# Optimization experiments

Hardware: AMD Instinct MI355X
Metric: run time of the kernel (lower is better)

## Reference

```python
import jax, jax.numpy as jnp
import numpy as np

N = 500000   # total atoms
M = 16384    # molecules (superatoms)
D = 256      # fingerprint_dim
EPS_BN = 1e-6
EPS_SM = 1e-8


def setup_inputs() -> dict:
    key = jax.random.key(0)
    ks = jax.random.split(key, 12)
    inp = {}
    inp['superatom'] = jax.random.normal(ks[0], (M, D), dtype=jnp.float32)
    inp['atom'] = jax.random.normal(ks[1], (N, D), dtype=jnp.float32)
    inp['mol_index'] = jnp.sort(jax.random.randint(ks[2], (N,), 0, M, dtype=jnp.int64))
    # align: Linear(2D, 1)
    inp['align_w'] = jax.random.normal(ks[3], (1, 2 * D), dtype=jnp.float32) / np.sqrt(2 * D)
    inp['align_b'] = jnp.zeros((1,), dtype=jnp.float32)
    # attend: LinearBn(D, D) -> linear + BatchNorm1d (eval mode, running stats)
    inp['attend_w'] = jax.random.normal(ks[4], (D, D), dtype=jnp.float32) / np.sqrt(D)
    inp['attend_b'] = jnp.zeros((D,), dtype=jnp.float32)
    inp['bn_gamma'] = jnp.ones((D,), dtype=jnp.float32)
    inp['bn_beta'] = jnp.zeros((D,), dtype=jnp.float32)
    inp['bn_mean'] = 0.01 * jax.random.normal(ks[5], (D,), dtype=jnp.float32)
    inp['bn_var'] = jnp.ones((D,), dtype=jnp.float32) + 0.01 * jax.random.uniform(ks[6], (D,), dtype=jnp.float32)
    # GRUCell(D, D): torch layout, gate order (r, z, n)
    inp['gru_wih'] = jax.random.normal(ks[7], (3 * D, D), dtype=jnp.float32) / np.sqrt(D)
    inp['gru_whh'] = jax.random.normal(ks[8], (3 * D, D), dtype=jnp.float32) / np.sqrt(D)
    inp['gru_bih'] = jnp.zeros((3 * D,), dtype=jnp.float32)
    inp['gru_bhh'] = jnp.zeros((3 * D,), dtype=jnp.float32)
    return inp


def _segment_softmax(x, index, num_segments):
    # x: [N,1], index: [N] -> segment-wise softmax (as in torch_scatter version)
    seg_max = jax.ops.segment_max(x, index, num_segments=num_segments)  # [M,1]
    seg_max = jnp.where(jnp.isfinite(seg_max), seg_max, 0.0)
    e = jnp.exp(x - seg_max[index])
    denom = jax.ops.segment_sum(e, index, num_segments=num_segments)  # [M,1]
    return e / (denom[index] + EPS_SM)


def _gru_cell(x, h, wih, whh, bih, bhh):
    gx = x @ wih.T + bih  # [M,3D]
    gh = h @ whh.T + bhh
    xr, xz, xn = jnp.split(gx, 3, axis=-1)
    hr, hz, hn = jnp.split(gh, 3, axis=-1)
    r = jax.nn.sigmoid(xr + hr)
    z = jax.nn.sigmoid(xz + hz)
    n = jnp.tanh(xn + r * hn)
    return (1.0 - z) * n + z * h


def reference(superatom, atom, mol_index, align_w, align_b, attend_w, attend_b,
              bn_gamma, bn_beta, bn_mean, bn_var, gru_wih, gru_whh, gru_bih, gru_bhh):
    # dropout is identity in eval mode
    superatom_expand = superatom[mol_index]                     # [N,D] gather
    feature_align = jnp.concatenate([superatom_expand, atom], axis=-1)  # [N,2D]
    align_score = jax.nn.leaky_relu(feature_align @ align_w.T + align_b, 0.01)  # [N,1]
    attention_weight = _segment_softmax(align_score, mol_index, M)      # [N,1]
    # attend = Linear + BatchNorm1d (eval)
    attended = atom @ attend_w.T + attend_b
    attended = bn_gamma * (attended - bn_mean) * jax.lax.rsqrt(bn_var + EPS_BN) + bn_beta
    context = jax.ops.segment_sum(attention_weight * attended, mol_index, num_segments=M)  # [M,D]
    context = jax.nn.elu(context)
    update = _gru_cell(context, superatom, gru_wih, gru_whh, gru_bih, gru_bhh)  # [M,D]
    return (update, attention_weight)
```

## Files before the change

kernel.cpp:

```cpp
#include <hip/hip_runtime.h>
#include <hip/hip_bf16.h>

#define D_DIM 256
#define EPS_BN 1e-6f
#define EPS_SM 1e-8f

typedef __bf16 bf16x8 __attribute__((ext_vector_type(8)));
typedef __bf16 bf16x4 __attribute__((ext_vector_type(4)));
typedef float  f32x4  __attribute__((ext_vector_type(4)));

__device__ __forceinline__ float wave_reduce_sum(float v) {
    #pragma unroll
    for (int off = 1; off < 64; off <<= 1) v += __shfl_xor(v, off);
    return v;
}

__device__ __forceinline__ float wave_reduce_max(float v) {
    #pragma unroll
    for (int off = 1; off < 64; off <<= 1) v = fmaxf(v, __shfl_xor(v, off));
    return v;
}

__device__ __forceinline__ float sigmoidf_(float x) {
    return 1.0f / (1.0f + __expf(-x));
}

__device__ __forceinline__ void cvt_region(const float* __restrict__ s,
                                           __bf16* __restrict__ d,
                                           int n4, int idx, int stride) {
    const float4* s4 = (const float4*)s;
    bf16x4* d4 = (bf16x4*)d;
    for (int i = idx; i < n4; i += stride) {
        float4 v = s4[i];
        bf16x4 o;
        o[0] = (__bf16)v.x; o[1] = (__bf16)v.y; o[2] = (__bf16)v.z; o[3] = (__bf16)v.w;
        d4[i] = o;
    }
}

__global__ __launch_bounds__(256) void k0_convert(
    const float* __restrict__ superatom, __bf16* __restrict__ sup_bf, int M,
    const float* __restrict__ align_w,   const float* __restrict__ align_b,
    float* __restrict__ cvec,
    const float* __restrict__ attend_w,  __bf16* __restrict__ aw_bf,  int n_aw,
    const float* __restrict__ wih,       __bf16* __restrict__ wih_bf, int n_wih,
    const float* __restrict__ whh,       __bf16* __restrict__ whh_bf, int n_whh)
{
    const int tid  = threadIdx.x;
    const int lane = tid & 63;
    const int gw   = (blockIdx.x * 256 + tid) >> 6;
    const int nw   = (gridDim.x * 256) >> 6;

    const float4 w1 = ((const float4*)align_w)[lane];
    const float  b0 = align_b[0];

    for (int m = gw; m < M; m += nw) {
        float4 s = ((const float4*)(superatom + (size_t)m * D_DIM))[lane];
        bf16x4 o;
        o[0] = (__bf16)s.x; o[1] = (__bf16)s.y; o[2] = (__bf16)s.z; o[3] = (__bf16)s.w;
        ((bf16x4*)sup_bf)[(size_t)m * 64 + lane] = o;
        float p = s.x * w1.x + s.y * w1.y + s.z * w1.z + s.w * w1.w;
        p = wave_reduce_sum(p);
        if (lane == 0) cvec[m] = p + b0;
    }

    const int idx    = blockIdx.x * 256 + tid;
    const int stride = gridDim.x * 256;
    cvt_region(attend_w, aw_bf,  n_aw / 4,  idx, stride);
    cvt_region(wih,      wih_bf, n_wih / 4, idx, stride);
    cvt_region(whh,      whh_bf, n_whh / 4, idx, stride);
}

__global__ __launch_bounds__(256) void k1_score(
    const float* __restrict__ atom,
    const int*   __restrict__ mol_index,
    const float* __restrict__ align_w,
    const float* __restrict__ cvec,
    float* __restrict__ att_out,
    int*   __restrict__ seg_start,
    int N, int M)
{
    const int lane = threadIdx.x & 63;
    const int gw   = (blockIdx.x * 256 + threadIdx.x) >> 6;
    const int nw   = (gridDim.x * 256) >> 6;

    const float4 wa = ((const float4*)(align_w + D_DIM))[lane];

    for (int r = gw; r < N; r += nw) {
        float4 a = ((const float4*)(atom + (size_t)r * D_DIM))[lane];
        float p = a.x * wa.x + a.y * wa.y + a.z * wa.z + a.w * wa.w;
        p = wave_reduce_sum(p);
        const int m = mol_index[r];
        float sc = cvec[m] + p;
        sc = sc > 0.0f ? sc : 0.01f * sc;
        if (lane == 0) {
            att_out[r] = sc;
            if (r == 0) {
                for (int mm = 0; mm <= m; ++mm) seg_start[mm] = 0;
            } else {
                const int mp = mol_index[r - 1];
                if (mp != m)
                    for (int mm = mp + 1; mm <= m; ++mm) seg_start[mm] = r;
            }
            if (r == N - 1) {
                for (int mm = m + 1; mm <= M; ++mm) seg_start[mm] = N;
            }
        }
    }
}

__global__ __launch_bounds__(256) void k1_ctx(
    const float* __restrict__ atom,
    const int*   __restrict__ seg_start,
    float* __restrict__ att,
    __bf16* __restrict__ ctxwn_bf,
    float* __restrict__ wsum)
{
    const int lane = threadIdx.x & 63;
    const int wid  = threadIdx.x >> 6;
    const int m    = blockIdx.x * 4 + wid;

    const int segs = seg_start[m];
    const int sege = seg_start[m + 1];

    float lmax = -3.4e38f;
    for (int i = segs + lane; i < sege; i += 64) lmax = fmaxf(lmax, att[i]);
    const float bmax = wave_reduce_max(lmax);
    float ls = 0.0f;
    for (int i = segs + lane; i < sege; i += 64) ls += __expf(att[i] - bmax);
    const float S   = wave_reduce_sum(ls);
    const float inv = 1.0f / (S + EPS_SM);
    if (lane == 0) wsum[m] = S * inv;

    float4 acc = make_float4(0.f, 0.f, 0.f, 0.f);
    for (int i = segs; i < sege; ++i) {
        const float w = __expf(att[i] - bmax) * inv;
        float4 a = ((const float4*)(atom + (size_t)i * D_DIM))[lane];
        acc.x = fmaf(w, a.x, acc.x);
        acc.y = fmaf(w, a.y, acc.y);
        acc.z = fmaf(w, a.z, acc.z);
        acc.w = fmaf(w, a.w, acc.w);
        if (lane == 0) att[i] = w;
    }

    bf16x4 o;
    o[0] = (__bf16)acc.x; o[1] = (__bf16)acc.y; o[2] = (__bf16)acc.z; o[3] = (__bf16)acc.w;
    ((bf16x4*)ctxwn_bf)[(size_t)m * 64 + lane] = o;
}

__global__ __launch_bounds__(256) void k2_context(
    const __bf16* __restrict__ A,
    const __bf16* __restrict__ W,
    const float* __restrict__ attend_b,
    const float* __restrict__ gamma_, const float* __restrict__ beta_,
    const float* __restrict__ mean_,  const float* __restrict__ var_,
    const float* __restrict__ wsum,
    __bf16* __restrict__ context_bf)
{
    const int tid  = threadIdx.x;
    const int wid  = tid >> 6;
    const int lane = tid & 63;
    const int quad = lane >> 4;
    const int r16  = lane & 15;
    const int m0   = blockIdx.x * 64;
    const int n0   = blockIdx.y * 64;

    const int arow = m0 + wid * 16 + r16;
    f32x4 acc[4] = {};

    #pragma unroll
    for (int ks = 0; ks < 8; ++ks) {
        const int ko = ks * 32 + quad * 8;
        bf16x8 af = *(const bf16x8*)&A[(size_t)arow * D_DIM + ko];
        #pragma unroll
        for (int t = 0; t < 4; ++t) {
            bf16x8 bf = *(const bf16x8*)&W[(size_t)(n0 + t * 16 + r16) * D_DIM + ko];
            acc[t] = __builtin_amdgcn_mfma_f32_16x16x32_bf16(af, bf, acc[t], 0, 0, 0);
        }
    }

    #pragma unroll
    for (int t = 0; t < 4; ++t) {
        const int col = n0 + t * 16 + r16;
        const float sc = gamma_[col] * rsqrtf(var_[col] + EPS_BN);
        const float cb = (attend_b[col] - mean_[col]) * sc + beta_[col];
        #pragma unroll
        for (int r = 0; r < 4; ++r) {
            const int row = m0 + wid * 16 + quad * 4 + r;
            float pre = acc[t][r] * sc + wsum[row] * cb;
            float e = pre > 0.0f ? pre : (__expf(pre) - 1.0f);
            context_bf[(size_t)row * D_DIM + col] = (__bf16)e;
        }
    }
}

__global__ __launch_bounds__(256) void k3_gru(
    const __bf16* __restrict__ ctx_bf,
    const __bf16* __restrict__ sup_bf,
    const float*  __restrict__ superatom,
    const __bf16* __restrict__ wih_bf,
    const __bf16* __restrict__ whh_bf,
    const float* __restrict__ bih,
    const float* __restrict__ bhh,
    float* __restrict__ out)
{
    const int tid  = threadIdx.x;
    const int wid  = tid >> 6;
    const int lane = tid & 63;
    const int quad = lane >> 4;
    const int r16  = lane & 15;
    const int m0   = blockIdx.x * 64;
    const int n0   = blockIdx.y * 64;

    const int arow = m0 + wid * 16 + r16;
    f32x4 acc[6][4] = {};

    #pragma unroll
    for (int ks = 0; ks < 8; ++ks) {
        const int ko = ks * 32 + quad * 8;
        bf16x8 ca = *(const bf16x8*)&ctx_bf[(size_t)arow * D_DIM + ko];
        bf16x8 ha = *(const bf16x8*)&sup_bf[(size_t)arow * D_DIM + ko];
        #pragma unroll
        for (int t = 0; t < 4; ++t) {
            const int brow = n0 + t * 16 + r16;
            bf16x8 b0 = *(const bf16x8*)&wih_bf[(size_t)(0 * D_DIM + brow) * D_DIM + ko];
            bf16x8 b1 = *(const bf16x8*)&wih_bf[(size_t)(1 * D_DIM + brow) * D_DIM + ko];
            bf16x8 b2 = *(const bf16x8*)&wih_bf[(size_t)(2 * D_DIM + brow) * D_DIM + ko];
            bf16x8 b3 = *(const bf16x8*)&whh_bf[(size_t)(0 * D_DIM + brow) * D_DIM + ko];
            bf16x8 b4 = *(const bf16x8*)&whh_bf[(size_t)(1 * D_DIM + brow) * D_DIM + ko];
            bf16x8 b5 = *(const bf16x8*)&whh_bf[(size_t)(2 * D_DIM + brow) * D_DIM + ko];
            acc[0][t] = __builtin_amdgcn_mfma_f32_16x16x32_bf16(ca, b0, acc[0][t], 0, 0, 0);
            acc[1][t] = __builtin_amdgcn_mfma_f32_16x16x32_bf16(ca, b1, acc[1][t], 0, 0, 0);
            acc[2][t] = __builtin_amdgcn_mfma_f32_16x16x32_bf16(ca, b2, acc[2][t], 0, 0, 0);
            acc[3][t] = __builtin_amdgcn_mfma_f32_16x16x32_bf16(ha, b3, acc[3][t], 0, 0, 0);
            acc[4][t] = __builtin_amdgcn_mfma_f32_16x16x32_bf16(ha, b4, acc[4][t], 0, 0, 0);
            acc[5][t] = __builtin_amdgcn_mfma_f32_16x16x32_bf16(ha, b5, acc[5][t], 0, 0, 0);
        }
    }

    #pragma unroll
    for (int t = 0; t < 4; ++t) {
        const int col = n0 + t * 16 + r16;
        const float br  = bih[col]             + bhh[col];
        const float bz  = bih[D_DIM + col]     + bhh[D_DIM + col];
        const float bxn = bih[2 * D_DIM + col];
        const float bhn = bhh[2 * D_DIM + col];
        #pragma unroll
        for (int r = 0; r < 4; ++r) {
            const int row = m0 + wid * 16 + quad * 4 + r;
            float rg = sigmoidf_(acc[0][t][r] + acc[3][t][r] + br);
            float z  = sigmoidf_(acc[1][t][r] + acc[4][t][r] + bz);
            float n  = tanhf(acc[2][t][r] + bxn + rg * (acc[5][t][r] + bhn));
            float h  = superatom[(size_t)row * D_DIM + col];
            out[(size_t)row * D_DIM + col] = (1.0f - z) * n + z * h;
        }
    }
}

extern "C" void kernel_launch(void* const* d_in, const int* in_sizes, int n_in,
                              void* d_out, int out_size, void* d_ws, size_t ws_size,
                              hipStream_t stream) {
    const float* superatom = (const float*)d_in[0];
    const float* atom      = (const float*)d_in[1];
    const int*   mol_index = (const int*)d_in[2];
    const float* align_w   = (const float*)d_in[3];
    const float* align_b   = (const float*)d_in[4];
    const float* attend_w  = (const float*)d_in[5];
    const float* attend_b  = (const float*)d_in[6];
    const float* bn_gamma  = (const float*)d_in[7];
    const float* bn_beta   = (const float*)d_in[8];
    const float* bn_mean   = (const float*)d_in[9];
    const float* bn_var    = (const float*)d_in[10];
    const float* gru_wih   = (const float*)d_in[11];
    const float* gru_whh   = (const float*)d_in[12];
    const float* gru_bih   = (const float*)d_in[13];
    const float* gru_bhh   = (const float*)d_in[14];

    const int M = in_sizes[0] / D_DIM;
    const int N = in_sizes[2];

    float* out     = (float*)d_out;
    float* att_out = out + (size_t)M * D_DIM;

    char* ws = (char*)d_ws;
    __bf16* ctxwn_bf   = (__bf16*)ws;                     ws += (size_t)M * D_DIM * 2;
    __bf16* context_bf = (__bf16*)ws;                     ws += (size_t)M * D_DIM * 2;
    __bf16* sup_bf     = (__bf16*)ws;                     ws += (size_t)M * D_DIM * 2;
    __bf16* aw_bf      = (__bf16*)ws;                     ws += (size_t)D_DIM * D_DIM * 2;
    __bf16* wih_bf     = (__bf16*)ws;                     ws += (size_t)3 * D_DIM * D_DIM * 2;
    __bf16* whh_bf     = (__bf16*)ws;                     ws += (size_t)3 * D_DIM * D_DIM * 2;
    float*  wsum       = (float*)ws;                      ws += (size_t)M * 4;
    float*  cvec       = (float*)ws;                      ws += (size_t)M * 4;
    int*    seg_start  = (int*)ws;                        ws += (size_t)(M + 1) * 4;

    k0_convert<<<M / 4, 256, 0, stream>>>(superatom, sup_bf, M,
                                          align_w, align_b, cvec,
                                          attend_w, aw_bf, D_DIM * D_DIM,
                                          gru_wih, wih_bf, 3 * D_DIM * D_DIM,
                                          gru_whh, whh_bf, 3 * D_DIM * D_DIM);
    k1_score<<<2048, 256, 0, stream>>>(atom, mol_index, align_w, cvec,
                                       att_out, seg_start, N, M);
    k1_ctx<<<M / 4, 256, 0, stream>>>(atom, seg_start, att_out, ctxwn_bf, wsum);
    k2_context<<<dim3(M / 64, D_DIM / 64), 256, 0, stream>>>(ctxwn_bf, aw_bf, attend_b,
                                                             bn_gamma, bn_beta, bn_mean, bn_var,
                                                             wsum, context_bf);
    k3_gru<<<dim3(M / 64, D_DIM / 64), 256, 0, stream>>>(context_bf, sup_bf, superatom,
                                                         wih_bf, whh_bf, gru_bih, gru_bhh,
                                                         out);
}
```

Before: 960.0 us.

## Fuse score and segment softmax-context into one online-softmax kernel per molecule

```diff
diff --git a/kernel.cpp b/kernel.cpp
--- a/kernel.cpp
+++ b/kernel.cpp
@@ -12,12 +12,6 @@
 __device__ __forceinline__ float wave_reduce_sum(float v) {
     #pragma unroll
     for (int off = 1; off < 64; off <<= 1) v += __shfl_xor(v, off);
-    return v;
-}
-
-__device__ __forceinline__ float wave_reduce_max(float v) {
-    #pragma unroll
-    for (int off = 1; off < 64; off <<= 1) v = fmaxf(v, __shfl_xor(v, off));
     return v;
 }
 
@@ -42,6 +36,7 @@
     const float* __restrict__ superatom, __bf16* __restrict__ sup_bf, int M,
     const float* __restrict__ align_w,   const float* __restrict__ align_b,
     float* __restrict__ cvec,
+    const int*   __restrict__ mol_index, int* __restrict__ seg_start, int N,
     const float* __restrict__ attend_w,  __bf16* __restrict__ aw_bf,  int n_aw,
     const float* __restrict__ wih,       __bf16* __restrict__ wih_bf, int n_wih,
     const float* __restrict__ whh,       __bf16* __restrict__ whh_bf, int n_whh)
@@ -69,83 +64,91 @@
     cvt_region(attend_w, aw_bf,  n_aw / 4,  idx, stride);
     cvt_region(wih,      wih_bf, n_wih / 4, idx, stride);
     cvt_region(whh,      whh_bf, n_whh / 4, idx, stride);
-}
-
-__global__ __launch_bounds__(256) void k1_score(
+
+    for (int i = idx; i < N; i += stride) {
+        const int m = mol_index[i];
+        if (i == 0) {
+            for (int mm = 0; mm <= m; ++mm) seg_start[mm] = 0;
+        } else {
+            const int mp = mol_index[i - 1];
+            if (mp != m)
+                for (int mm = mp + 1; mm <= m; ++mm) seg_start[mm] = i;
+        }
+        if (i == N - 1) {
+            for (int mm = m + 1; mm <= M; ++mm) seg_start[mm] = N;
+        }
+    }
+}
+
+__global__ __launch_bounds__(256) void k1_segment(
     const float* __restrict__ atom,
-    const int*   __restrict__ mol_index,
     const float* __restrict__ align_w,
     const float* __restrict__ cvec,
+    const int*   __restrict__ seg_start,
+    __bf16* __restrict__ ctxwn_bf,
+    float* __restrict__ wsum,
     float* __restrict__ att_out,
-    int*   __restrict__ seg_start,
-    int N, int M)
+    int N)
 {
-    const int lane = threadIdx.x & 63;
-    const int gw   = (blockIdx.x * 256 + threadIdx.x) >> 6;
-    const int nw   = (gridDim.x * 256) >> 6;
-
+    const int m    = blockIdx.x;
+    const int tid  = threadIdx.x;
+    const int wid  = tid >> 6;
+    const int lane = tid & 63;
+
+    const int segs = seg_start[m];
+    const int sege = seg_start[m + 1];
+
+    const float cm = cvec[m];
     const float4 wa = ((const float4*)(align_w + D_DIM))[lane];
 
-    for (int r = gw; r < N; r += nw) {
-        float4 a = ((const float4*)(atom + (size_t)r * D_DIM))[lane];
+    __shared__ float smax[4];
+    __shared__ float ssum[4];
+    __shared__ float sacc[4 * D_DIM];
+
+    float m_run = -3.4e38f;
+    float S = 0.0f;
+    float4 acc = make_float4(0.f, 0.f, 0.f, 0.f);
+    for (int i = segs + wid; i < sege; i += 4) {
+        float4 a = ((const float4*)(atom + (size_t)i * D_DIM))[lane];
         float p = a.x * wa.x + a.y * wa.y + a.z * wa.z + a.w * wa.w;
         p = wave_reduce_sum(p);
-        const int m = mol_index[r];
-        float sc = cvec[m] + p;
+        float sc = cm + p;
         sc = sc > 0.0f ? sc : 0.01f * sc;
-        if (lane == 0) {
-            att_out[r] = sc;
-            if (r == 0) {
-                for (int mm = 0; mm <= m; ++mm) seg_start[mm] = 0;
-            } else {
-                const int mp = mol_index[r - 1];
-                if (mp != m)
-                    for (int mm = mp + 1; mm <= m; ++mm) seg_start[mm] = r;
-            }
-            if (r == N - 1) {
-                for (int mm = m + 1; mm <= M; ++mm) seg_start[mm] = N;
-            }
-        }
-    }
-}
-
-__global__ __launch_bounds__(256) void k1_ctx(
-    const float* __restrict__ atom,
-    const int*   __restrict__ seg_start,
-    float* __restrict__ att,
-    __bf16* __restrict__ ctxwn_bf,
-    float* __restrict__ wsum)
-{
-    const int lane = threadIdx.x & 63;
-    const int wid  = threadIdx.x >> 6;
-    const int m    = blockIdx.x * 4 + wid;
-
-    const int segs = seg_start[m];
-    const int sege = seg_start[m + 1];
-
-    float lmax = -3.4e38f;
-    for (int i = segs + lane; i < sege; i += 64) lmax = fmaxf(lmax, att[i]);
-    const float bmax = wave_reduce_max(lmax);
-    float ls = 0.0f;
-    for (int i = segs + lane; i < sege; i += 64) ls += __expf(att[i] - bmax);
-    const float S   = wave_reduce_sum(ls);
-    const float inv = 1.0f / (S + EPS_SM);
-    if (lane == 0) wsum[m] = S * inv;
-
-    float4 acc = make_float4(0.f, 0.f, 0.f, 0.f);
-    for (int i = segs; i < sege; ++i) {
-        const float w = __expf(att[i] - bmax) * inv;
-        float4 a = ((const float4*)(atom + (size_t)i * D_DIM))[lane];
-        acc.x = fmaf(w, a.x, acc.x);
-        acc.y = fmaf(w, a.y, acc.y);
-        acc.z = fmaf(w, a.z, acc.z);
-        acc.w = fmaf(w, a.w, acc.w);
-        if (lane == 0) att[i] = w;
-    }
-
-    bf16x4 o;
-    o[0] = (__bf16)acc.x; o[1] = (__bf16)acc.y; o[2] = (__bf16)acc.z; o[3] = (__bf16)acc.w;
-    ((bf16x4*)ctxwn_bf)[(size_t)m * 64 + lane] = o;
+        if (lane == 0) att_out[i] = sc;
+        if (sc <= m_run) {
+            float e = __expf(sc - m_run);
+            S += e;
+            acc.x = fmaf(e, a.x, acc.x); acc.y = fmaf(e, a.y, acc.y);
+            acc.z = fmaf(e, a.z, acc.z); acc.w = fmaf(e, a.w, acc.w);
+        } else {
+            float corr = __expf(m_run - sc);
+            S = fmaf(S, corr, 1.0f);
+            acc.x = fmaf(acc.x, corr, a.x); acc.y = fmaf(acc.y, corr, a.y);
+            acc.z = fmaf(acc.z, corr, a.z); acc.w = fmaf(acc.w, corr, a.w);
+            m_run = sc;
+        }
+    }
+    if (lane == 0) smax[wid] = m_run;
+    __syncthreads();
+    const float bmax = fmaxf(fmaxf(smax[0], smax[1]), fmaxf(smax[2], smax[3]));
+    {
+        float corr = __expf(m_run - bmax);
+        S *= corr;
+        acc.x *= corr; acc.y *= corr; acc.z *= corr; acc.w *= corr;
+    }
+    ((float4*)sacc)[wid * 64 + lane] = acc;
+    if (lane == 0) ssum[wid] = S;
+    __syncthreads();
+
+    const float Stot = ssum[0] + ssum[1] + ssum[2] + ssum[3];
+    const float inv  = 1.0f / (Stot + EPS_SM);
+    float v = sacc[tid] + sacc[D_DIM + tid] + sacc[2 * D_DIM + tid] + sacc[3 * D_DIM + tid];
+    ctxwn_bf[(size_t)m * D_DIM + tid] = (__bf16)(v * inv);
+    if (tid == 0) wsum[m] = Stot * inv;
+
+    for (int i = segs + tid; i < sege; i += 256) {
+        att_out[i] = __expf(att_out[i] - bmax) * inv;
+    }
 }
 
 __global__ __launch_bounds__(256) void k2_context(
@@ -295,12 +298,12 @@
 
     k0_convert<<<M / 4, 256, 0, stream>>>(superatom, sup_bf, M,
                                           align_w, align_b, cvec,
+                                          mol_index, seg_start, N,
                                           attend_w, aw_bf, D_DIM * D_DIM,
                                           gru_wih, wih_bf, 3 * D_DIM * D_DIM,
                                           gru_whh, whh_bf, 3 * D_DIM * D_DIM);
-    k1_score<<<2048, 256, 0, stream>>>(atom, mol_index, align_w, cvec,
-                                       att_out, seg_start, N, M);
-    k1_ctx<<<M / 4, 256, 0, stream>>>(atom, seg_start, att_out, ctxwn_bf, wsum);
+    k1_segment<<<M, 256, 0, stream>>>(atom, align_w, cvec, seg_start,
+                                      ctxwn_bf, wsum, att_out, N);
     k2_context<<<dim3(M / 64, D_DIM / 64), 256, 0, stream>>>(ctxwn_bf, aw_bf, attend_b,
                                                              bn_gamma, bn_beta, bn_mean, bn_var,
                                                              wsum, context_bf);
```

New measurement: 823.1 us. 14.3% less time.
